# Performance work log

Hardware: AMD Instinct MI355X
Metric: run time of the kernel (lower is better)

## Reference

```python
import jax, jax.numpy as jnp
import numpy as np

TEMP = 0.2
LAM = 0.5
EPS = 1e-8

N, IN_SIZE, HID = 8192, 256, 128


def setup_inputs() -> dict:
    key = jax.random.key(0)
    k1, k2, k3, k4, k5 = jax.random.split(key, 5)
    z_mp = jax.random.normal(k1, (N, IN_SIZE), dtype=jnp.float32)
    z_sc = jax.random.normal(k2, (N, IN_SIZE), dtype=jnp.float32)
    # xavier-normal-ish init scale
    W1 = jax.random.normal(k3, (IN_SIZE, HID), dtype=jnp.float32) * (1.414 * (2.0 / (IN_SIZE + HID)) ** 0.5)
    b1 = jnp.zeros((HID,), dtype=jnp.float32)
    W2 = jax.random.normal(k4, (HID, HID), dtype=jnp.float32) * (1.414 * (2.0 / (HID + HID)) ** 0.5)
    b2 = jnp.zeros((HID,), dtype=jnp.float32)
    pos = jax.random.randint(k5, (N, N), 0, 2, dtype=jnp.int32)
    return {"z_mp": z_mp, "z_sc": z_sc, "W1": W1, "b1": b1, "W2": W2, "b2": b2, "pos": pos}


def _proj(z, W1, b1, W2, b2):
    # Linear -> ELU -> Linear
    return jax.nn.elu(z @ W1 + b1) @ W2 + b2


def _l2norm(z):
    # F.normalize(p=2, dim=1): torch uses clamp_min(eps) on the norm
    n = jnp.linalg.norm(z, axis=1, keepdims=True)
    return z / jnp.maximum(n, 1e-12)


def reference(z_mp, z_sc, W1, b1, W2, b2, pos):
    zp_sc = _proj(z_sc, W1, b1, W2, b2)
    zp_mp = _proj(z_mp, W1, b1, W2, b2)
    # exp(cosine similarity / temperature), dense N x N
    sim = jnp.exp(_l2norm(zp_mp) @ _l2norm(zp_sc).T / TEMP)  # [N, N] mp2sc
    mp2sc = sim / (jnp.sum(sim, axis=1, keepdims=True) + EPS)
    sc2mp = sim.T / (jnp.sum(sim, axis=0)[:, None] + EPS)
    posf = pos.astype(sim.dtype)
    lori_sc = -jnp.log(jnp.sum(sc2mp * posf, axis=-1) + EPS)
    lori_mp = -jnp.log(jnp.sum(mp2sc * posf, axis=-1) + EPS)
    ans = LAM * lori_mp + (1.0 - LAM) * lori_sc
    ans = jnp.where(jnp.isnan(ans) | jnp.isinf(ans), jnp.zeros((), ans.dtype), ans)
    return ans
```

## Files before the change

kernel.cpp:

```cpp
#include <hip/hip_runtime.h>
#include <math.h>

#define N_ROWS 8192
#define IN_SZ 256
#define HID 128
#define INV_TEMP 5.0f
#define EPSV 1e-8f

typedef short short8 __attribute__((ext_vector_type(8)));
typedef float f32x4 __attribute__((ext_vector_type(4)));

__device__ __forceinline__ ushort f2bf(float v) {
    unsigned b = __float_as_uint(v);
    return (ushort)((b + 0x7FFFu + ((b >> 16) & 1u)) >> 16);
}
__device__ __forceinline__ float bf2f(ushort u) {
    return __uint_as_float(((unsigned)u) << 16);
}

__global__ __launch_bounds__(256) void pack_kernel(
    const int* __restrict__ pos, unsigned* __restrict__ posbits,
    float* __restrict__ sums)
{
    const int t = threadIdx.x;
    if (blockIdx.x < 4) {
        float4 z4 = make_float4(0.f, 0.f, 0.f, 0.f);
        float* base = sums + (size_t)blockIdx.x * 8192 + t * 32;
#pragma unroll
        for (int i = 0; i < 8; ++i) *(float4*)(base + i * 4) = z4;
    }
    const size_t nthreads = (size_t)gridDim.x * 256;
    const size_t total_groups = (size_t)N_ROWS * N_ROWS / 4;
    for (size_t g = (size_t)blockIdx.x * 256 + t; g < total_groups; g += nthreads) {
        int4 v = *(const int4*)(pos + g * 4);
        unsigned nib = (v.x != 0 ? 1u : 0u) | (v.y != 0 ? 2u : 0u)
                     | (v.z != 0 ? 4u : 0u) | (v.w != 0 ? 8u : 0u);
        unsigned u = nib << ((t & 7) * 4);
        u |= (unsigned)__shfl_xor((int)u, 1);
        u |= (unsigned)__shfl_xor((int)u, 2);
        u |= (unsigned)__shfl_xor((int)u, 4);
        if ((t & 7) == 0) posbits[g >> 3] = u;
    }
}

__global__ __launch_bounds__(256) void proj_kernel(
    const float* __restrict__ z_mp, const float* __restrict__ z_sc,
    const float* __restrict__ W1, const float* __restrict__ b1,
    const float* __restrict__ W2, const float* __restrict__ b2,
    ushort* __restrict__ h_mp, ushort* __restrict__ l_mp,
    ushort* __restrict__ h_sc, ushort* __restrict__ l_sc)
{
    __shared__ float smem[10368];
    float* sZ  = smem;
    float* sW  = smem + 2176;
    float* sH  = smem;
    float* sW2 = smem + 4224;
    float* snorm = smem + 8320;

    const int t = threadIdx.x;
    const int sel = blockIdx.y;
    const int R0 = blockIdx.x * 32;
    const int tx = t & 15, ty = t >> 4;
    const float* z = (sel == 0) ? z_mp : z_sc;
    ushort* outH   = (sel == 0) ? h_mp : h_sc;
    ushort* outL   = (sel == 0) ? l_mp : l_sc;

    if (t < 32) snorm[t] = 0.f;

    float acc[2][8];
#pragma unroll
    for (int i = 0; i < 2; ++i)
#pragma unroll
        for (int j = 0; j < 8; ++j) acc[i][j] = 0.f;

    for (int ch = 0; ch < 4; ++ch) {
#pragma unroll
        for (int it = 0; it < 2; ++it) {
            int idx = it * 256 + t;
            int k4 = idx >> 5;
            int m  = idx & 31;
            float4 v = *(const float4*)(z + (size_t)(R0 + m) * IN_SZ + ch * 64 + k4 * 4);
            sZ[(k4 * 4 + 0) * 34 + m] = v.x;
            sZ[(k4 * 4 + 1) * 34 + m] = v.y;
            sZ[(k4 * 4 + 2) * 34 + m] = v.z;
            sZ[(k4 * 4 + 3) * 34 + m] = v.w;
        }
#pragma unroll
        for (int it = 0; it < 8; ++it) {
            int idx = it * 256 + t;
            int kk = idx >> 5;
            int c4 = idx & 31;
            *(float4*)(sW + kk * 128 + c4 * 4) =
                *(const float4*)(W1 + (size_t)(ch * 64 + kk) * HID + c4 * 4);
        }
        __syncthreads();
#pragma unroll 4
        for (int k = 0; k < 64; ++k) {
            float2 a = *(const float2*)(sZ + k * 34 + ty * 2);
            float4 b0 = *(float4*)(sW + k * 128 + tx * 4);
            float4 b1v = *(float4*)(sW + k * 128 + 64 + tx * 4);
            float av[2] = {a.x, a.y};
            float bv[8] = {b0.x, b0.y, b0.z, b0.w, b1v.x, b1v.y, b1v.z, b1v.w};
#pragma unroll
            for (int i = 0; i < 2; ++i)
#pragma unroll
                for (int j = 0; j < 8; ++j)
                    acc[i][j] = fmaf(av[i], bv[j], acc[i][j]);
        }
        __syncthreads();
    }

#pragma unroll
    for (int j = 0; j < 8; ++j) {
        int c = (j < 4) ? tx * 4 + j : 64 + tx * 4 + (j - 4);
        float bb = b1[c];
#pragma unroll
        for (int i = 0; i < 2; ++i) {
            float v = acc[i][j] + bb;
            v = (v > 0.f) ? v : (__expf(v) - 1.f);
            sH[c * 33 + ty * 2 + i] = v;
        }
    }

    float acc2[2][8];
#pragma unroll
    for (int i = 0; i < 2; ++i)
#pragma unroll
        for (int j = 0; j < 8; ++j) acc2[i][j] = 0.f;

    for (int ch2 = 0; ch2 < 4; ++ch2) {
#pragma unroll
        for (int it = 0; it < 4; ++it) {
            int idx = it * 256 + t;
            int kk = idx >> 5;
            int c4 = idx & 31;
            *(float4*)(sW2 + kk * 128 + c4 * 4) =
                *(const float4*)(W2 + (size_t)(ch2 * 32 + kk) * HID + c4 * 4);
        }
        __syncthreads();
#pragma unroll 4
        for (int k2 = 0; k2 < 32; ++k2) {
            float a0 = sH[(ch2 * 32 + k2) * 33 + ty * 2];
            float a1 = sH[(ch2 * 32 + k2) * 33 + ty * 2 + 1];
            float4 b0 = *(float4*)(sW2 + k2 * 128 + tx * 4);
            float4 b1v = *(float4*)(sW2 + k2 * 128 + 64 + tx * 4);
            float av[2] = {a0, a1};
            float bv[8] = {b0.x, b0.y, b0.z, b0.w, b1v.x, b1v.y, b1v.z, b1v.w};
#pragma unroll
            for (int i = 0; i < 2; ++i)
#pragma unroll
                for (int j = 0; j < 8; ++j)
                    acc2[i][j] = fmaf(av[i], bv[j], acc2[i][j]);
        }
        __syncthreads();
    }

#pragma unroll
    for (int j = 0; j < 8; ++j) {
        int c = (j < 4) ? tx * 4 + j : 64 + tx * 4 + (j - 4);
        float bb = b2[c];
#pragma unroll
        for (int i = 0; i < 2; ++i) acc2[i][j] += bb;
    }
#pragma unroll
    for (int i = 0; i < 2; ++i) {
        float p = 0.f;
#pragma unroll
        for (int j = 0; j < 8; ++j) p = fmaf(acc2[i][j], acc2[i][j], p);
        atomicAdd(&snorm[ty * 2 + i], p);
    }
    __syncthreads();
#pragma unroll
    for (int i = 0; i < 2; ++i) {
        int r = ty * 2 + i;
        float scale = 1.f / fmaxf(sqrtf(snorm[r]), 1e-12f);
#pragma unroll
        for (int half = 0; half < 2; ++half) {
            ushort4 h4, l4;
            ushort hu[4], lu[4];
#pragma unroll
            for (int j = 0; j < 4; ++j) {
                float v = acc2[i][half * 4 + j] * scale;
                ushort hb = f2bf(v);
                float lv = v - bf2f(hb);
                hu[j] = hb;
                lu[j] = f2bf(lv);
            }
            h4.x = hu[0]; h4.y = hu[1]; h4.z = hu[2]; h4.w = hu[3];
            l4.x = lu[0]; l4.y = lu[1]; l4.z = lu[2]; l4.w = lu[3];
            size_t off = (size_t)(R0 + r) * HID + half * 64 + tx * 4;
            *(ushort4*)(outH + off) = h4;
            *(ushort4*)(outL + off) = l4;
        }
    }
}

__global__ __launch_bounds__(256, 3) void sim_mfma_kernel(
    const ushort* __restrict__ mh_, const ushort* __restrict__ ml_,
    const ushort* __restrict__ sh_, const ushort* __restrict__ sl_,
    const unsigned* __restrict__ posbits, float* __restrict__ sums)
{
    __shared__ float redR[128], redRP[128], redC[128], redCP[128];
    __shared__ float tbuf[4][16 * 68];
    __shared__ unsigned sBR[128][4];
    __shared__ unsigned sBC[128][4];

    const int t = threadIdx.x;
    const int lane = t & 63;
    const int wave = t >> 6;
    const int wr = wave >> 1, wc = wave & 1;
    const int I = blockIdx.y * 128;
    const int J = blockIdx.x * 128;
    const int r0 = wr * 64, c0 = wc * 64;
    const int lrow = lane & 15;
    const int quad = lane >> 4;

    if (t < 128) {
        redR[t] = 0.f; redRP[t] = 0.f;
        *(uint4*)sBR[t] = *(const uint4*)(posbits + (size_t)(I + t) * (N_ROWS / 32) + J / 32);
    } else {
        int u = t - 128;
        redC[u] = 0.f; redCP[u] = 0.f;
        *(uint4*)sBC[u] = *(const uint4*)(posbits + (size_t)(J + u) * (N_ROWS / 32) + I / 32);
    }
    __syncthreads();

    const short* mh = (const short*)mh_;
    const short* ml = (const short*)ml_;
    const short* sh = (const short*)sh_;
    const short* sl = (const short*)sl_;

    unsigned aoff[4], boff[4];
#pragma unroll
    for (int s = 0; s < 4; ++s) {
        aoff[s] = (unsigned)(I + r0 + s * 16 + lrow) * HID + quad * 8;
        boff[s] = (unsigned)(J + c0 + s * 16 + lrow) * HID + quad * 8;
    }

    f32x4 acc[4][4];
#pragma unroll
    for (int si = 0; si < 4; ++si)
#pragma unroll
        for (int sj = 0; sj < 4; ++sj) acc[si][sj] = (f32x4)0.f;

#pragma unroll 1
    for (int ks = 0; ks < 4; ++ks) {
        const unsigned ko = ks * 32;
        short8 ah[4], bh[4];
#pragma unroll
        for (int s = 0; s < 4; ++s) {
            ah[s] = *(const short8*)(mh + aoff[s] + ko);
            bh[s] = *(const short8*)(sh + boff[s] + ko);
        }
#pragma unroll
        for (int si = 0; si < 4; ++si)
#pragma unroll
            for (int sj = 0; sj < 4; ++sj)
                acc[si][sj] = __builtin_amdgcn_mfma_f32_16x16x32_bf16(
                    ah[si], bh[sj], acc[si][sj], 0, 0, 0);

        short8 bl[4];
#pragma unroll
        for (int s = 0; s < 4; ++s) bl[s] = *(const short8*)(sl + boff[s] + ko);
#pragma unroll
        for (int si = 0; si < 4; ++si)
#pragma unroll
            for (int sj = 0; sj < 4; ++sj)
                acc[si][sj] = __builtin_amdgcn_mfma_f32_16x16x32_bf16(
                    ah[si], bl[sj], acc[si][sj], 0, 0, 0);

        short8 al[4];
#pragma unroll
        for (int s = 0; s < 4; ++s) al[s] = *(const short8*)(ml + aoff[s] + ko);
#pragma unroll
        for (int si = 0; si < 4; ++si)
#pragma unroll
            for (int sj = 0; sj < 4; ++sj)
                acc[si][sj] = __builtin_amdgcn_mfma_f32_16x16x32_bf16(
                    al[si], bh[sj], acc[si][sj], 0, 0, 0);
    }

#pragma unroll
    for (int si = 0; si < 4; ++si)
#pragma unroll
        for (int sj = 0; sj < 4; ++sj)
#pragma unroll
            for (int r = 0; r < 4; ++r)
                acc[si][sj][r] = __expf(acc[si][sj][r] * INV_TEMP);

#pragma unroll
    for (int sj = 0; sj < 4; ++sj) {
        int n = c0 + sj * 16 + lrow;
        float cs = 0.f, cp = 0.f;
#pragma unroll
        for (int si = 0; si < 4; ++si) {
            f32x4 v = acc[si][sj];
            cs += v[0] + v[1] + v[2] + v[3];
            int bb = r0 + si * 16 + quad * 4;
            unsigned bits = (sBC[n][bb >> 5] >> (bb & 31)) & 0xF;
            cp += (bits & 1u ? v[0] : 0.f) + (bits & 2u ? v[1] : 0.f)
                + (bits & 4u ? v[2] : 0.f) + (bits & 8u ? v[3] : 0.f);
        }
        cs += __shfl_xor(cs, 16); cs += __shfl_xor(cs, 32);
        cp += __shfl_xor(cp, 16); cp += __shfl_xor(cp, 32);
        if (lane < 16) {
            atomicAdd(&redC[c0 + sj * 16 + lane], cs);
            atomicAdd(&redCP[c0 + sj * 16 + lane], cp);
        }
    }

    float* tw = tbuf[wave];
#pragma unroll
    for (int si = 0; si < 4; ++si) {
#pragma unroll
        for (int sj = 0; sj < 4; ++sj)
#pragma unroll
            for (int r = 0; r < 4; ++r)
                tw[(quad * 4 + r) * 68 + sj * 16 + lrow] = acc[si][sj][r];
        int row = lane & 15;
        int chunk = lane >> 4;
        const unsigned prw = sBR[r0 + si * 16 + row][(c0 >> 5) + (chunk >> 1)];
        float rs = 0.f, rp = 0.f;
#pragma unroll
        for (int c4 = 0; c4 < 4; ++c4) {
            f32x4 v = *(const f32x4*)(tw + row * 68 + chunk * 16 + c4 * 4);
            unsigned bits = (prw >> ((chunk & 1) * 16 + c4 * 4)) & 0xF;
            rs += v[0] + v[1] + v[2] + v[3];
            rp += (bits & 1u ? v[0] : 0.f) + (bits & 2u ? v[1] : 0.f)
                + (bits & 4u ? v[2] : 0.f) + (bits & 8u ? v[3] : 0.f);
        }
        rs += __shfl_xor(rs, 16); rs += __shfl_xor(rs, 32);
        rp += __shfl_xor(rp, 16); rp += __shfl_xor(rp, 32);
        if (lane < 16) {
            atomicAdd(&redR[r0 + si * 16 + lane], rs);
            atomicAdd(&redRP[r0 + si * 16 + lane], rp);
        }
    }
    __syncthreads();

    if (t < 128) {
        atomicAdd(&sums[I + t],              redR[t]);
        atomicAdd(&sums[N_ROWS + I + t],     redRP[t]);
        atomicAdd(&sums[2 * N_ROWS + J + t], redC[t]);
        atomicAdd(&sums[3 * N_ROWS + J + t], redCP[t]);
    }
}

__global__ __launch_bounds__(256) void finish_kernel(
    const float* __restrict__ sums, float* __restrict__ out)
{
    int i = blockIdx.x * 256 + threadIdx.x;
    if (i >= N_ROWS) return;
    float rsv = sums[i];
    float rpv = sums[N_ROWS + i];
    float csv = sums[2 * N_ROWS + i];
    float cpv = sums[3 * N_ROWS + i];
    float lmp = -logf(rpv / (rsv + EPSV) + EPSV);
    float lsc = -logf(cpv / (csv + EPSV) + EPSV);
    float a = 0.5f * lmp + 0.5f * lsc;
    if (!isfinite(a)) a = 0.f;
    out[i] = a;
}

extern "C" void kernel_launch(void* const* d_in, const int* in_sizes, int n_in,
                              void* d_out, int out_size, void* d_ws, size_t ws_size,
                              hipStream_t stream) {
    const float* z_mp = (const float*)d_in[0];
    const float* z_sc = (const float*)d_in[1];
    const float* W1   = (const float*)d_in[2];
    const float* b1   = (const float*)d_in[3];
    const float* W2   = (const float*)d_in[4];
    const float* b2   = (const float*)d_in[5];
    const int*   pos  = (const int*)d_in[6];
    float* out = (float*)d_out;

    ushort* wsu = (ushort*)d_ws;
    const size_t NV = (size_t)N_ROWS * HID;
    ushort* mh = wsu;
    ushort* ml = wsu + NV;
    ushort* sh = wsu + 2 * NV;
    ushort* sl = wsu + 3 * NV;
    float* sums = (float*)(wsu + 4 * NV);
    unsigned* posbits = (unsigned*)(sums + 4 * N_ROWS);

    pack_kernel<<<2048, 256, 0, stream>>>(pos, posbits, sums);
    proj_kernel<<<dim3(256, 2), 256, 0, stream>>>(
        z_mp, z_sc, W1, b1, W2, b2, mh, ml, sh, sl);
    sim_mfma_kernel<<<dim3(64, 64), 256, 0, stream>>>(mh, ml, sh, sl, posbits, sums);
    finish_kernel<<<N_ROWS / 256, 256, 0, stream>>>(sums, out);
}
```

Measured before the change: 528.8 us.

## Double-buffer MFMA operand loads and defer pos-bit LDS staging past GEMM

The sim kernel's K loop becomes fully unrolled with two register buffer sets, so global loads for the next K slice are issued while the MFMAs for the current slice run. The pos-bit tile load is started up front into a register and only written to shared memory after the GEMM and exp, which drops the early barrier. The launch-bounds occupancy hint of 3 is removed, since the doubled operand registers would not fit under it. The pack kernel loop also gets an unroll-4 pragma. The cost is much higher register pressure, which may lower occupancy or cause spills.

```diff
diff --git a/kernel.cpp b/kernel.cpp
--- a/kernel.cpp
+++ b/kernel.cpp
@@ -31,6 +31,7 @@
     }
     const size_t nthreads = (size_t)gridDim.x * 256;
     const size_t total_groups = (size_t)N_ROWS * N_ROWS / 4;
+#pragma unroll 4
     for (size_t g = (size_t)blockIdx.x * 256 + t; g < total_groups; g += nthreads) {
         int4 v = *(const int4*)(pos + g * 4);
         unsigned nib = (v.x != 0 ? 1u : 0u) | (v.y != 0 ? 2u : 0u)
@@ -195,7 +196,36 @@
     }
 }
 
-__global__ __launch_bounds__(256, 3) void sim_mfma_kernel(
+__device__ __forceinline__ void load4(short8 (&dst)[4], const short* __restrict__ base,
+                                      const unsigned (&off)[4], int ko) {
+#pragma unroll
+    for (int s = 0; s < 4; ++s) dst[s] = *(const short8*)(base + off[s] + ko);
+}
+
+__device__ __forceinline__ void mfma3(f32x4 (&acc)[4][4], const short8 (&ah)[4],
+                                      const short8 (&bh)[4], const short8 (&bl)[4],
+                                      const short8 (&al)[4]) {
+#pragma unroll
+    for (int si = 0; si < 4; ++si)
+#pragma unroll
+        for (int sj = 0; sj < 4; ++sj)
+            acc[si][sj] = __builtin_amdgcn_mfma_f32_16x16x32_bf16(
+                ah[si], bh[sj], acc[si][sj], 0, 0, 0);
+#pragma unroll
+    for (int si = 0; si < 4; ++si)
+#pragma unroll
+        for (int sj = 0; sj < 4; ++sj)
+            acc[si][sj] = __builtin_amdgcn_mfma_f32_16x16x32_bf16(
+                ah[si], bl[sj], acc[si][sj], 0, 0, 0);
+#pragma unroll
+    for (int si = 0; si < 4; ++si)
+#pragma unroll
+        for (int sj = 0; sj < 4; ++sj)
+            acc[si][sj] = __builtin_amdgcn_mfma_f32_16x16x32_bf16(
+                al[si], bh[sj], acc[si][sj], 0, 0, 0);
+}
+
+__global__ __launch_bounds__(256) void sim_mfma_kernel(
     const ushort* __restrict__ mh_, const ushort* __restrict__ ml_,
     const ushort* __restrict__ sh_, const ushort* __restrict__ sl_,
     const unsigned* __restrict__ posbits, float* __restrict__ sums)
@@ -215,15 +245,9 @@
     const int lrow = lane & 15;
     const int quad = lane >> 4;
 
-    if (t < 128) {
-        redR[t] = 0.f; redRP[t] = 0.f;
-        *(uint4*)sBR[t] = *(const uint4*)(posbits + (size_t)(I + t) * (N_ROWS / 32) + J / 32);
-    } else {
-        int u = t - 128;
-        redC[u] = 0.f; redCP[u] = 0.f;
-        *(uint4*)sBC[u] = *(const uint4*)(posbits + (size_t)(J + u) * (N_ROWS / 32) + I / 32);
-    }
-    __syncthreads();
+    uint4 pb;
+    if (t < 128) pb = *(const uint4*)(posbits + (size_t)(I + t) * (N_ROWS / 32) + J / 32);
+    else         pb = *(const uint4*)(posbits + (size_t)(J + t - 128) * (N_ROWS / 32) + I / 32);
 
     const short* mh = (const short*)mh_;
     const short* ml = (const short*)ml_;
@@ -243,42 +267,21 @@
 #pragma unroll
         for (int sj = 0; sj < 4; ++sj) acc[si][sj] = (f32x4)0.f;
 
-#pragma unroll 1
-    for (int ks = 0; ks < 4; ++ks) {
-        const unsigned ko = ks * 32;
-        short8 ah[4], bh[4];
-#pragma unroll
-        for (int s = 0; s < 4; ++s) {
-            ah[s] = *(const short8*)(mh + aoff[s] + ko);
-            bh[s] = *(const short8*)(sh + boff[s] + ko);
-        }
-#pragma unroll
-        for (int si = 0; si < 4; ++si)
-#pragma unroll
-            for (int sj = 0; sj < 4; ++sj)
-                acc[si][sj] = __builtin_amdgcn_mfma_f32_16x16x32_bf16(
-                    ah[si], bh[sj], acc[si][sj], 0, 0, 0);
-
-        short8 bl[4];
-#pragma unroll
-        for (int s = 0; s < 4; ++s) bl[s] = *(const short8*)(sl + boff[s] + ko);
-#pragma unroll
-        for (int si = 0; si < 4; ++si)
-#pragma unroll
-            for (int sj = 0; sj < 4; ++sj)
-                acc[si][sj] = __builtin_amdgcn_mfma_f32_16x16x32_bf16(
-                    ah[si], bl[sj], acc[si][sj], 0, 0, 0);
-
-        short8 al[4];
-#pragma unroll
-        for (int s = 0; s < 4; ++s) al[s] = *(const short8*)(ml + aoff[s] + ko);
-#pragma unroll
-        for (int si = 0; si < 4; ++si)
-#pragma unroll
-            for (int sj = 0; sj < 4; ++sj)
-                acc[si][sj] = __builtin_amdgcn_mfma_f32_16x16x32_bf16(
-                    al[si], bh[sj], acc[si][sj], 0, 0, 0);
-    }
+    short8 ahA[4], bhA[4], blA[4], alA[4];
+    short8 ahB[4], bhB[4], blB[4], alB[4];
+
+    load4(ahA, mh, aoff, 0);  load4(bhA, sh, boff, 0);
+    load4(blA, sl, boff, 0);  load4(alA, ml, aoff, 0);
+    load4(ahB, mh, aoff, 32); load4(bhB, sh, boff, 32);
+    load4(blB, sl, boff, 32); load4(alB, ml, aoff, 32);
+    mfma3(acc, ahA, bhA, blA, alA);
+    load4(ahA, mh, aoff, 64); load4(bhA, sh, boff, 64);
+    load4(blA, sl, boff, 64); load4(alA, ml, aoff, 64);
+    mfma3(acc, ahB, bhB, blB, alB);
+    load4(ahB, mh, aoff, 96); load4(bhB, sh, boff, 96);
+    load4(blB, sl, boff, 96); load4(alB, ml, aoff, 96);
+    mfma3(acc, ahA, bhA, blA, alA);
+    mfma3(acc, ahB, bhB, blB, alB);
 
 #pragma unroll
     for (int si = 0; si < 4; ++si)
@@ -287,6 +290,16 @@
 #pragma unroll
             for (int r = 0; r < 4; ++r)
                 acc[si][sj][r] = __expf(acc[si][sj][r] * INV_TEMP);
+
+    if (t < 128) {
+        redR[t] = 0.f; redRP[t] = 0.f;
+        *(uint4*)sBR[t] = pb;
+    } else {
+        int u = t - 128;
+        redC[u] = 0.f; redCP[u] = 0.f;
+        *(uint4*)sBC[u] = pb;
+    }
+    __syncthreads();
 
 #pragma unroll
     for (int sj = 0; sj < 4; ++sj) {
```

Result: slower. 563.6 us (+6.6%).

## Stage bf16 operand tiles through LDS with direct global-to-LDS loads

Applied to the files above, without the earlier changes.

The similarity MFMA kernel now stages each 32-wide K slice of the hi/lo A and B operands into shared memory using global_load_lds, with an XOR swizzle to avoid bank conflicts. Previously every wave loaded its own fragments straight from global memory, so the same rows were fetched redundantly across waves. The transpose scratch buffer now reuses the staging area, and the posbits load is issued early into registers so its latency overlaps the GEMM. The pack kernel loop also gets an unroll pragma. The cost is extra barriers per K step, a larger shared-memory footprint (32KB), and no double buffering, so loads and MFMAs do not overlap. The larger LDS use may reduce occupancy.

```diff
diff --git a/kernel.cpp b/kernel.cpp
--- a/kernel.cpp
+++ b/kernel.cpp
@@ -16,6 +16,12 @@
 }
 __device__ __forceinline__ float bf2f(ushort u) {
     return __uint_as_float(((unsigned)u) << 16);
+}
+
+__device__ __forceinline__ void gl2lds16(const void* g, void* l) {
+    __builtin_amdgcn_global_load_lds(
+        (const __attribute__((address_space(1))) unsigned*)g,
+        (__attribute__((address_space(3))) unsigned*)l, 16, 0, 0);
 }
 
 __global__ __launch_bounds__(256) void pack_kernel(
@@ -31,6 +37,7 @@
     }
     const size_t nthreads = (size_t)gridDim.x * 256;
     const size_t total_groups = (size_t)N_ROWS * N_ROWS / 4;
+#pragma unroll 8
     for (size_t g = (size_t)blockIdx.x * 256 + t; g < total_groups; g += nthreads) {
         int4 v = *(const int4*)(pos + g * 4);
         unsigned nib = (v.x != 0 ? 1u : 0u) | (v.y != 0 ? 2u : 0u)
@@ -201,9 +208,9 @@
     const unsigned* __restrict__ posbits, float* __restrict__ sums)
 {
     __shared__ float redR[128], redRP[128], redC[128], redCP[128];
-    __shared__ float tbuf[4][16 * 68];
     __shared__ unsigned sBR[128][4];
     __shared__ unsigned sBC[128][4];
+    __shared__ __align__(16) char stage[32768];
 
     const int t = threadIdx.x;
     const int lane = t & 63;
@@ -215,78 +222,105 @@
     const int lrow = lane & 15;
     const int quad = lane >> 4;
 
+    uint4 pb;
+    if (t < 128) pb = *(const uint4*)(posbits + (size_t)(I + t) * (N_ROWS / 32) + J / 32);
+    else         pb = *(const uint4*)(posbits + (size_t)(J + t - 128) * (N_ROWS / 32) + I / 32);
+
+    const char* mhB = (const char*)mh_;
+    const char* mlB = (const char*)ml_;
+    const char* shB = (const char*)sh_;
+    const char* slB = (const char*)sl_;
+
+    const int rsub = lane >> 2;
+    const int cfetch = (lane & 3) ^ ((lane >> 3) & 3);
+    const size_t ga0 = (size_t)(I + wave * 32 + rsub) * 256 + cfetch * 16;
+    const size_t ga1 = ga0 + 16 * 256;
+    const size_t gb0 = (size_t)(J + wave * 32 + rsub) * 256 + cfetch * 16;
+    const size_t gb1 = gb0 + 16 * 256;
+    char* sAh = stage;
+    char* sAl = stage + 8192;
+    char* sBh = stage + 16384;
+    char* sBl = stage + 24576;
+    const unsigned ls0 = wave * 2048, ls1 = ls0 + 1024;
+
+    const int slot = quad ^ ((lrow >> 1) & 3);
+    unsigned ra[4], rb[4];
+#pragma unroll
+    for (int s = 0; s < 4; ++s) {
+        ra[s] = (unsigned)(r0 + s * 16 + lrow) * 64 + slot * 16;
+        rb[s] = (unsigned)(c0 + s * 16 + lrow) * 64 + slot * 16;
+    }
+
+    f32x4 acc[4][4];
+#pragma unroll
+    for (int si = 0; si < 4; ++si)
+#pragma unroll
+        for (int sj = 0; sj < 4; ++sj) acc[si][sj] = (f32x4)0.f;
+
+#pragma unroll
+    for (int ks = 0; ks < 4; ++ks) {
+        const unsigned kb = ks * 64;
+        if (ks) __syncthreads();
+        gl2lds16(mhB + ga0 + kb, sAh + ls0);
+        gl2lds16(mhB + ga1 + kb, sAh + ls1);
+        gl2lds16(mlB + ga0 + kb, sAl + ls0);
+        gl2lds16(mlB + ga1 + kb, sAl + ls1);
+        gl2lds16(shB + gb0 + kb, sBh + ls0);
+        gl2lds16(shB + gb1 + kb, sBh + ls1);
+        gl2lds16(slB + gb0 + kb, sBl + ls0);
+        gl2lds16(slB + gb1 + kb, sBl + ls1);
+        __syncthreads();
+
+        short8 ah[4], bh[4];
+#pragma unroll
+        for (int s = 0; s < 4; ++s) ah[s] = *(const short8*)(sAh + ra[s]);
+#pragma unroll
+        for (int s = 0; s < 4; ++s) bh[s] = *(const short8*)(sBh + rb[s]);
+#pragma unroll
+        for (int si = 0; si < 4; ++si)
+#pragma unroll
+            for (int sj = 0; sj < 4; ++sj)
+                acc[si][sj] = __builtin_amdgcn_mfma_f32_16x16x32_bf16(
+                    ah[si], bh[sj], acc[si][sj], 0, 0, 0);
+
+        short8 bl[4];
+#pragma unroll
+        for (int s = 0; s < 4; ++s) bl[s] = *(const short8*)(sBl + rb[s]);
+#pragma unroll
+        for (int si = 0; si < 4; ++si)
+#pragma unroll
+            for (int sj = 0; sj < 4; ++sj)
+                acc[si][sj] = __builtin_amdgcn_mfma_f32_16x16x32_bf16(
+                    ah[si], bl[sj], acc[si][sj], 0, 0, 0);
+
+        short8 al[4];
+#pragma unroll
+        for (int s = 0; s < 4; ++s) al[s] = *(const short8*)(sAl + ra[s]);
+#pragma unroll
+        for (int si = 0; si < 4; ++si)
+#pragma unroll
+            for (int sj = 0; sj < 4; ++sj)
+                acc[si][sj] = __builtin_amdgcn_mfma_f32_16x16x32_bf16(
+                    al[si], bh[sj], acc[si][sj], 0, 0, 0);
+    }
+
+#pragma unroll
+    for (int si = 0; si < 4; ++si)
+#pragma unroll
+        for (int sj = 0; sj < 4; ++sj)
+#pragma unroll
+            for (int r = 0; r < 4; ++r)
+                acc[si][sj][r] = __expf(acc[si][sj][r] * INV_TEMP);
+
     if (t < 128) {
         redR[t] = 0.f; redRP[t] = 0.f;
-        *(uint4*)sBR[t] = *(const uint4*)(posbits + (size_t)(I + t) * (N_ROWS / 32) + J / 32);
+        *(uint4*)sBR[t] = pb;
     } else {
         int u = t - 128;
         redC[u] = 0.f; redCP[u] = 0.f;
-        *(uint4*)sBC[u] = *(const uint4*)(posbits + (size_t)(J + u) * (N_ROWS / 32) + I / 32);
+        *(uint4*)sBC[u] = pb;
     }
     __syncthreads();
-
-    const short* mh = (const short*)mh_;
-    const short* ml = (const short*)ml_;
-    const short* sh = (const short*)sh_;
-    const short* sl = (const short*)sl_;
-
-    unsigned aoff[4], boff[4];
-#pragma unroll
-    for (int s = 0; s < 4; ++s) {
-        aoff[s] = (unsigned)(I + r0 + s * 16 + lrow) * HID + quad * 8;
-        boff[s] = (unsigned)(J + c0 + s * 16 + lrow) * HID + quad * 8;
-    }
-
-    f32x4 acc[4][4];
-#pragma unroll
-    for (int si = 0; si < 4; ++si)
-#pragma unroll
-        for (int sj = 0; sj < 4; ++sj) acc[si][sj] = (f32x4)0.f;
-
-#pragma unroll 1
-    for (int ks = 0; ks < 4; ++ks) {
-        const unsigned ko = ks * 32;
-        short8 ah[4], bh[4];
-#pragma unroll
-        for (int s = 0; s < 4; ++s) {
-            ah[s] = *(const short8*)(mh + aoff[s] + ko);
-            bh[s] = *(const short8*)(sh + boff[s] + ko);
-        }
-#pragma unroll
-        for (int si = 0; si < 4; ++si)
-#pragma unroll
-            for (int sj = 0; sj < 4; ++sj)
-                acc[si][sj] = __builtin_amdgcn_mfma_f32_16x16x32_bf16(
-                    ah[si], bh[sj], acc[si][sj], 0, 0, 0);
-
-        short8 bl[4];
-#pragma unroll
-        for (int s = 0; s < 4; ++s) bl[s] = *(const short8*)(sl + boff[s] + ko);
-#pragma unroll
-        for (int si = 0; si < 4; ++si)
-#pragma unroll
-            for (int sj = 0; sj < 4; ++sj)
-                acc[si][sj] = __builtin_amdgcn_mfma_f32_16x16x32_bf16(
-                    ah[si], bl[sj], acc[si][sj], 0, 0, 0);
-
-        short8 al[4];
-#pragma unroll
-        for (int s = 0; s < 4; ++s) al[s] = *(const short8*)(ml + aoff[s] + ko);
-#pragma unroll
-        for (int si = 0; si < 4; ++si)
-#pragma unroll
-            for (int sj = 0; sj < 4; ++sj)
-                acc[si][sj] = __builtin_amdgcn_mfma_f32_16x16x32_bf16(
-                    al[si], bh[sj], acc[si][sj], 0, 0, 0);
-    }
-
-#pragma unroll
-    for (int si = 0; si < 4; ++si)
-#pragma unroll
-        for (int sj = 0; sj < 4; ++sj)
-#pragma unroll
-            for (int r = 0; r < 4; ++r)
-                acc[si][sj][r] = __expf(acc[si][sj][r] * INV_TEMP);
 
 #pragma unroll
     for (int sj = 0; sj < 4; ++sj) {
@@ -309,7 +343,7 @@
         }
     }
 
-    float* tw = tbuf[wave];
+    float* tw = (float*)(stage + wave * 4352);
 #pragma unroll
     for (int si = 0; si < 4; ++si) {
 #pragma unroll
```

Measured after the change: 482.6 us. 1.1x faster.
